# Optimization experiments

Hardware: AMD Instinct MI355X
Metric: run time of the kernel (lower is better)

## Reference

```python
import jax, jax.numpy as jnp
import numpy as np
from jax import lax

EPS = 1e-8

def _cosine_cost(x, y):
    # 1 - cosine_similarity over feature dim: [B,N,M]
    xn = x / jnp.clip(jnp.linalg.norm(x, axis=-1, keepdims=True), EPS)
    yn = y / jnp.clip(jnp.linalg.norm(y, axis=-1, keepdims=True), EPS)
    return 1.0 - jnp.einsum('bnd,bmd->bnm', xn, yn)

def _dtw_table(cost):
    # cost: [B,N,M] -> cumulative cost tc: [B,N,M]
    # tc[i,j] = cost[i,j] + min(tc[i-1,j-1], tc[i-1,j], tc[i,j-1])
    B, N, M = cost.shape
    row0 = jnp.cumsum(cost[:, 0, :], axis=1)  # [B,M]

    def col_step(left, inp):
        c, pdiag, pup = inp  # each [B]
        v = c + jnp.minimum(jnp.minimum(pdiag, pup), left)
        return v, v

    def row_step(prev, cost_row):
        # prev, cost_row: [B,M]
        first = prev[:, 0] + cost_row[:, 0]  # [B]
        xs = (cost_row[:, 1:].T, prev[:, :-1].T, prev[:, 1:].T)  # [M-1,B]
        _, rest = lax.scan(col_step, first, xs)  # [M-1,B]
        row = jnp.concatenate([first[:, None], rest.T], axis=1)  # [B,M]
        return row, row

    _, rows = lax.scan(row_step, row0, jnp.swapaxes(cost[:, 1:, :], 0, 1))
    tc = jnp.concatenate([row0[:, None, :], jnp.swapaxes(rows, 0, 1)], axis=1)
    return tc

def _backtrack(tc):
    # tc: [N,M] -> 0/1 path matrix [N,M]; tie-break diag > up > left,
    # matching the torch equality-chain order.
    N, M = tc.shape
    path0 = jnp.zeros((N, M), tc.dtype).at[N - 1, M - 1].set(1.0)

    def cond(s):
        i, j, _ = s
        return jnp.logical_and(i > 0, j > 0)

    def body(s):
        i, j, p = s
        a = tc[i - 1, j - 1]
        b = tc[i - 1, j]
        c = tc[i, j - 1]
        diag = jnp.logical_and(a <= b, a <= c)
        up = jnp.logical_and(jnp.logical_not(diag), b <= c)
        ni = jnp.where(jnp.logical_or(diag, up), i - 1, i)
        nj = jnp.where(jnp.logical_or(diag, jnp.logical_not(up)), j - 1, j)
        p = p.at[ni, nj].set(1.0)
        return ni, nj, p

    _, _, p = lax.while_loop(cond, body, (jnp.int32(N - 1), jnp.int32(M - 1), path0))
    return p.at[0, 0].set(1.0)

def setup_inputs() -> dict:
    key = jax.random.key(0)
    kx, ky = jax.random.split(key)
    B, N, M, D = 64, 512, 512, 256
    x = jax.random.normal(kx, (B, N, D), dtype=jnp.float32)
    y = jax.random.normal(ky, (B, M, D), dtype=jnp.float32)
    return {"x": x, "y": y}

def reference(x, y):
    cost = _cosine_cost(x, y)                 # [B,N,M]
    tc = _dtw_table(cost)                     # [B,N,M]
    path = jax.vmap(_backtrack)(tc)           # [B,N,M]
    pos = jax.nn.logsumexp(jnp.sum(cost * path, axis=1), axis=1)  # [B]
    neg = jax.nn.logsumexp(jnp.sum(cost, axis=1), axis=1)         # [B]
    return pos - neg
```

## Files before the change

### kernel.cpp

```cpp
#include <hip/hip_runtime.h>
#include <hip/hip_bf16.h>
#include <stdint.h>

typedef __attribute__((ext_vector_type(8))) short short8v;
typedef __attribute__((ext_vector_type(4))) float float4v;
typedef __attribute__((ext_vector_type(4))) unsigned short ushort4v;
typedef __attribute__((ext_vector_type(4))) unsigned int uint4v;

#define FINF __builtin_huge_valf()
#define BB 64
#define NN 512
#define DD 256
#define TT_SKEW 576


static __device__ __forceinline__ unsigned short f2bf(float f) {
  union { float f; uint32_t u; } a; a.f = f;
  uint32_t r = a.u + 0x7fffu + ((a.u >> 16) & 1u);
  return (unsigned short)(r >> 16);
}
static __device__ __forceinline__ float bf2f(uint16_t v) {
  return __uint_as_float(((uint32_t)v) << 16);
}

__global__ __launch_bounds__(64) void pad_zero_kernel(uint16_t* __restrict__ skew)
{
  const int bid = blockIdx.x;
  const int b = bid >> 7, k = bid & 127;
  const int t   = (k < 64) ? k : (448 + k);
  const int jlo = (k < 64) ? 8 * (t + 1) : 0;
  const int jhi = (k < 64) ? 512 : 8 * (t - 511);
  uint16_t* p = skew + ((size_t)b * TT_SKEW + t) * NN;
  const int j = jlo + (int)threadIdx.x * 8;
  if (j < jhi) *(uint4v*)(p + j) = (uint4v){0u, 0u, 0u, 0u};
}

__global__ __launch_bounds__(256) void norm_cast_kernel(
    const float* __restrict__ x, const float* __restrict__ y,
    uint16_t* __restrict__ xnb, uint16_t* __restrict__ ynb)
{
  const int wave = threadIdx.x >> 6, lane = threadIdx.x & 63;
  const int row = blockIdx.x * 4 + wave;
  const float* src; uint16_t* dst;
  if (row < BB * NN) { src = x + (size_t)row * DD;            dst = xnb + (size_t)row * DD; }
  else               { src = y + (size_t)(row - BB*NN) * DD;  dst = ynb + (size_t)(row - BB*NN) * DD; }
  const float4v v = *(const float4v*)(src + lane * 4);
  float s = v[0]*v[0] + v[1]*v[1] + v[2]*v[2] + v[3]*v[3];
  #pragma unroll
  for (int d = 1; d < 64; d <<= 1) s += __shfl_xor(s, d, 64);
  const float inv = 1.0f / fmaxf(sqrtf(s), 1e-8f);
  ushort4v o;
  o[0] = f2bf(v[0] * inv); o[1] = f2bf(v[1] * inv);
  o[2] = f2bf(v[2] * inv); o[3] = f2bf(v[3] * inv);
  *(ushort4v*)(dst + lane * 4) = o;
}

__global__ __launch_bounds__(256) void gemm_cost_kernel(
    const uint16_t* __restrict__ xnb, const uint16_t* __restrict__ ynb,
    uint16_t* __restrict__ skew)
{
  __shared__ uint16_t As[128 * 32];
  __shared__ uint16_t Bs[128 * 32];
  const int bid = blockIdx.x;
  const int b = bid >> 4, tm = (bid >> 2) & 3, tn = bid & 3;
  const int tid = threadIdx.x, wave = tid >> 6, lane = tid & 63;
  const int wr = wave >> 1, wc = wave & 1;

  const char* Ab = (const char*)(xnb + (size_t)b * NN * DD + (size_t)tm * 128 * DD);
  const char* Bb = (const char*)(ynb + (size_t)b * NN * DD + (size_t)tn * 128 * DD);

  float4v acc[4][4];
  #pragma unroll
  for (int i = 0; i < 4; i++)
    #pragma unroll
    for (int j = 0; j < 4; j++) acc[i][j] = (float4v){0.f, 0.f, 0.f, 0.f};

  const int seg0 = wave * 2;
  const int o0 = seg0 * 1024 + lane * 16;
  const int o1 = o0 + 1024;
  const int r0 = o0 >> 6, c0 = o0 & 63;
  const int r1 = o1 >> 6, c1 = o1 & 63;

  for (int kk = 0; kk < 8; kk++) {
    const int kb = kk * 64;
    __builtin_amdgcn_global_load_lds(
        (const __attribute__((address_space(1))) uint32_t*)(Ab + (size_t)r0 * 512 + kb + c0),
        (__attribute__((address_space(3))) uint32_t*)((char*)As + seg0 * 1024), 16, 0, 0);
    __builtin_amdgcn_global_load_lds(
        (const __attribute__((address_space(1))) uint32_t*)(Ab + (size_t)r1 * 512 + kb + c1),
        (__attribute__((address_space(3))) uint32_t*)((char*)As + (seg0 + 1) * 1024), 16, 0, 0);
    __builtin_amdgcn_global_load_lds(
        (const __attribute__((address_space(1))) uint32_t*)(Bb + (size_t)r0 * 512 + kb + c0),
        (__attribute__((address_space(3))) uint32_t*)((char*)Bs + seg0 * 1024), 16, 0, 0);
    __builtin_amdgcn_global_load_lds(
        (const __attribute__((address_space(1))) uint32_t*)(Bb + (size_t)r1 * 512 + kb + c1),
        (__attribute__((address_space(3))) uint32_t*)((char*)Bs + (seg0 + 1) * 1024), 16, 0, 0);
    __syncthreads();

    short8v af[4], bfr[4];
    #pragma unroll
    for (int mi = 0; mi < 4; mi++) {
      const int rr = wr * 64 + mi * 16 + (lane & 15);
      af[mi] = *(const short8v*)((const char*)As + rr * 64 + (lane >> 4) * 16);
    }
    #pragma unroll
    for (int nj = 0; nj < 4; nj++) {
      const int rr = wc * 64 + nj * 16 + (lane & 15);
      bfr[nj] = *(const short8v*)((const char*)Bs + rr * 64 + (lane >> 4) * 16);
    }
    #pragma unroll
    for (int mi = 0; mi < 4; mi++)
      #pragma unroll
      for (int nj = 0; nj < 4; nj++)
        acc[mi][nj] = __builtin_amdgcn_mfma_f32_16x16x32_bf16(af[mi], bfr[nj], acc[mi][nj], 0, 0, 0);
    __syncthreads();
  }

  uint16_t* Cb = skew + (size_t)b * TT_SKEW * NN;
  #pragma unroll
  for (int mi = 0; mi < 4; mi++)
    #pragma unroll
    for (int nj = 0; nj < 4; nj++) {
      const int cc = tn * 128 + wc * 64 + nj * 16 + (lane & 15);
      const int lg = cc >> 3;
      #pragma unroll
      for (int v = 0; v < 4; v++) {
        const int rr = tm * 128 + wr * 64 + mi * 16 + (lane >> 4) * 4 + v;
        Cb[(size_t)(rr + lg) * NN + cc] = f2bf(1.0f - acc[mi][nj][v]);
      }
    }
}

__global__ __launch_bounds__(256) void neg_lse_kernel(
    const uint16_t* __restrict__ skew, float* __restrict__ negbuf)
{
  __shared__ float sm[8];
  const int b = blockIdx.x, tid = threadIdx.x;
  const int wave = tid >> 6, lane = tid & 63;
  const uint32_t* p = (const uint32_t*)(skew + (size_t)b * TT_SKEW * NN) + tid;
  float s0 = 0.f, s1 = 0.f;
  #pragma unroll 8
  for (int t = 0; t < TT_SKEW; ++t) {
    const uint32_t w = p[t * 256];
    s0 += __uint_as_float(w << 16);
    s1 += __uint_as_float(w & 0xFFFF0000u);
  }
  float m = fmaxf(s0, s1);
  #pragma unroll
  for (int d = 1; d < 64; d <<= 1) m = fmaxf(m, __shfl_xor(m, d, 64));
  if (lane == 0) sm[wave] = m;
  __syncthreads();
  m = fmaxf(fmaxf(sm[0], sm[1]), fmaxf(sm[2], sm[3]));
  float e = expf(s0 - m) + expf(s1 - m);
  #pragma unroll
  for (int d = 1; d < 64; d <<= 1) e += __shfl_xor(e, d, 64);
  if (lane == 0) sm[4 + wave] = e;
  __syncthreads();
  if (tid == 0) negbuf[b] = m + logf(sm[4] + sm[5] + sm[6] + sm[7]);
}

__global__ __launch_bounds__(64, 1) void dtw_kernel(
    const uint16_t* __restrict__ skew, const float* __restrict__ negbuf,
    float* __restrict__ out)
{
  extern __shared__ char lds_raw[];
  const int l = threadIdx.x;
  const int b = blockIdx.x;
  const uint16_t* csk = skew + (size_t)b * TT_SKEW * NN;
  const uint64_t base = (uint64_t)(uintptr_t)csk;

  uint32_t voff = 16u * (uint32_t)l;
  const uint32_t voff_max = 16u * (uint32_t)l + 575u * 1024u;

  uint4v ring[8];
  #pragma unroll
  for (int i = 0; i < 8; ++i) {
    asm volatile("global_load_dwordx4 %0, %1, %2"
                 : "=v"(ring[i]) : "v"(voff), "s"(base) : "memory");
    voff += 1024u;
  }

  float tprev[8];
  #pragma unroll
  for (int c = 0; c < 8; ++c) tprev[c] = FINF;
  float sh_p_carry = FINF, cur_last = FINF;
  uint32_t rlane = (uint32_t)(0 - l);
  const uint32_t lane_dec = ((uint32_t)l) << 2;
  const uint32_t dump_addr = 69632u + (((uint32_t)l) << 1);

  for (int t = 0; t < TT_SKEW; t += 8) {
    #pragma unroll
    for (int u = 0; u < 8; ++u) {
      const int tt = t + u;
      asm volatile("s_waitcnt vmcnt(7)" ::: "memory");
      __builtin_amdgcn_sched_barrier(0);
      const uint4v cur = ring[u];

      float sh_c = __shfl_up(cur_last, 1, 64);
      float sh_p = sh_p_carry;
      if (l == 0) { sh_p = FINF; sh_c = (tt == 0) ? 0.0f : FINF; }
      sh_p_carry = sh_c;
      const bool valid = (rlane < 512u);

      float S[8];
      {
        float c0 = __uint_as_float(cur[0] << 16);
        float c1 = __uint_as_float(cur[0] & 0xFFFF0000u);
        float c2 = __uint_as_float(cur[1] << 16);
        float c3 = __uint_as_float(cur[1] & 0xFFFF0000u);
        float c4 = __uint_as_float(cur[2] << 16);
        float c5 = __uint_as_float(cur[2] & 0xFFFF0000u);
        float c6 = __uint_as_float(cur[3] << 16);
        float c7 = __uint_as_float(cur[3] & 0xFFFF0000u);
        S[0] = c0; S[1] = S[0] + c1; S[2] = S[1] + c2; S[3] = S[2] + c3;
        S[4] = S[3] + c4; S[5] = S[4] + c5; S[6] = S[5] + c6; S[7] = S[6] + c7;
      }
      float dcp[8];
      dcp[0] = sh_p;
      #pragma unroll
      for (int c = 1; c < 8; ++c) dcp[c] = tprev[c - 1];
      float w8[8], PW[8];
      w8[0] = fminf(dcp[0], tprev[0]);
      #pragma unroll
      for (int c = 1; c < 8; ++c) w8[c] = fminf(dcp[c], tprev[c]) - S[c - 1];
      PW[0] = w8[0];
      #pragma unroll
      for (int c = 1; c < 8; ++c) PW[c] = fminf(PW[c - 1], w8[c]);
      float tnv[8];
      #pragma unroll
      for (int c = 0; c < 8; ++c) tnv[c] = fminf(PW[c], sh_c) + S[c];
      float lc[8];
      lc[0] = sh_c;
      #pragma unroll
      for (int c = 1; c < 8; ++c) lc[c] = tnv[c - 1];
      uint32_t word = 0;
      #pragma unroll
      for (int c = 0; c < 8; ++c) {
        const bool diag = dcp[c] <= fminf(tprev[c], lc[c]);
        const uint32_t dd = diag ? 0u : ((tprev[c] <= lc[c]) ? 1u : 2u);
        word |= dd << (2 * c);
      }
      const uint32_t wbyte = ((rlane & ~1u) << 7) | ((rlane & 1u) << 1) | lane_dec;
      const uint32_t waddr = valid ? wbyte : dump_addr;
      *(uint16_t*)(lds_raw + waddr) = (uint16_t)word;
      #pragma unroll
      for (int c = 0; c < 8; ++c) tprev[c] = valid ? tnv[c] : tprev[c];
      cur_last = tprev[7];
      rlane += 1u;

      asm volatile("global_load_dwordx4 %0, %1, %2"
                   : "=v"(ring[u]) : "v"(voff), "s"(base) : "memory");
      voff += 1024u;
      if (voff > voff_max) voff = voff_max;
    }
  }
  asm volatile("s_waitcnt vmcnt(0)" ::: "memory");
  __builtin_amdgcn_sched_barrier(0);

  uint16_t* rlo    = (uint16_t*)(lds_raw + 65536);
  uint16_t* rhi    = (uint16_t*)(lds_raw + 66560);
  float*    colpos = (float*)  (lds_raw + 67584);
  const uint32_t* dec32 = (const uint32_t*)lds_raw;

  for (int r = l; r < NN; r += 64) { rlo[r] = 1; rhi[r] = 0; colpos[r] = 0.0f; }
  __syncthreads();
  if (l == 0) {
    int i = NN - 1, j = NN - 1, hicur = NN - 1;
    int cidx = -1; uint32_t cw = 0;
    while (i > 0 && j > 0) {
      const int widx = (i >> 1) * 64 + (j >> 3);
      if (widx != cidx) { cw = dec32[widx]; cidx = widx; }
      const uint32_t dd = (cw >> (((i & 1) << 4) + ((j & 7) << 1))) & 3u;
      if (dd == 2u) { j--; }
      else {
        rlo[i] = (uint16_t)j; rhi[i] = (uint16_t)hicur;
        i--;
        if (dd == 0u) j--;
        hicur = j;
      }
    }
    rlo[i] = (uint16_t)j; rhi[i] = (uint16_t)hicur;
  }
  __syncthreads();
  for (int r = l; r < NN; r += 64) {
    const int lo = rlo[r], hi = rhi[r];
    for (int j = lo; j <= hi; j++) {
      const float cv = bf2f(csk[(size_t)(r + (j >> 3)) * NN + j]);
      atomicAdd(&colpos[j], cv);
    }
  }
  if (l == 0 && rlo[0] != 0) atomicAdd(&colpos[0], bf2f(csk[0]));
  __syncthreads();

  float mv[8];
  float mx2 = -FINF;
  #pragma unroll
  for (int k = 0; k < 8; k++) { mv[k] = colpos[l + 64 * k]; mx2 = fmaxf(mx2, mv[k]); }
  #pragma unroll
  for (int d = 1; d < 64; d <<= 1) mx2 = fmaxf(mx2, __shfl_xor(mx2, d, 64));
  float se2 = 0.f;
  #pragma unroll
  for (int k = 0; k < 8; k++) se2 += expf(mv[k] - mx2);
  #pragma unroll
  for (int d = 1; d < 64; d <<= 1) se2 += __shfl_xor(se2, d, 64);
  const float pos = mx2 + logf(se2);

  if (l == 0) out[b] = pos - negbuf[b];
}

extern "C" void kernel_launch(void* const* d_in, const int* in_sizes, int n_in,
                              void* d_out, int out_size, void* d_ws, size_t ws_size,
                              hipStream_t stream)
{
  (void)in_sizes; (void)n_in; (void)out_size; (void)ws_size;
  const float* x = (const float*)d_in[0];
  const float* y = (const float*)d_in[1];
  float* out = (float*)d_out;
  char* ws = (char*)d_ws;
  uint16_t* xnb  = (uint16_t*)ws;
  uint16_t* ynb  = (uint16_t*)(ws + (size_t)16777216);
  uint16_t* skew = (uint16_t*)(ws + (size_t)33554432);
  float*  negbuf = (float*)  (ws + (size_t)71303168);

  (void)hipFuncSetAttribute((const void*)dtw_kernel,
                            hipFuncAttributeMaxDynamicSharedMemorySize, 69888);

  pad_zero_kernel<<<8192, 64, 0, stream>>>(skew);
  norm_cast_kernel<<<16384, 256, 0, stream>>>(x, y, xnb, ynb);
  gemm_cost_kernel<<<1024, 256, 0, stream>>>(xnb, ynb, skew);
  neg_lse_kernel<<<64, 256, 0, stream>>>(skew, negbuf);
  dtw_kernel<<<64, 64, 69888, stream>>>(skew, negbuf, out);
}
```

Baseline: 292.6 us.

## Split DTW wavefront across two waves with four columns per lane

The DTW wavefront kernel now runs 128 threads per batch, each lane owning 4 columns instead of 8. The second wave lags by 8 diagonal steps and takes its left boundary from a handoff array in LDS written by lane 63 of the first wave. The cost skew layout changes to match: a shift of 4 columns per row, 640 skewed rows, and updated padding, GEMM store, decision-bit packing and backtrack indexing. The aim is a shorter serial dependency chain per diagonal step. In exchange it adds more diagonal steps and a block barrier every four steps.

```diff
diff --git a/kernel.cpp b/kernel.cpp
--- a/kernel.cpp
+++ b/kernel.cpp
@@ -6,12 +6,13 @@
 typedef __attribute__((ext_vector_type(4))) float float4v;
 typedef __attribute__((ext_vector_type(4))) unsigned short ushort4v;
 typedef __attribute__((ext_vector_type(4))) unsigned int uint4v;
+typedef __attribute__((ext_vector_type(2))) unsigned int uint2v;
 
 #define FINF __builtin_huge_valf()
 #define BB 64
 #define NN 512
 #define DD 256
-#define TT_SKEW 576
+#define TT_SKEW 640
 
 
 static __device__ __forceinline__ unsigned short f2bf(float f) {
@@ -26,13 +27,13 @@
 __global__ __launch_bounds__(64) void pad_zero_kernel(uint16_t* __restrict__ skew)
 {
   const int bid = blockIdx.x;
-  const int b = bid >> 7, k = bid & 127;
-  const int t   = (k < 64) ? k : (448 + k);
-  const int jlo = (k < 64) ? 8 * (t + 1) : 0;
-  const int jhi = (k < 64) ? 512 : 8 * (t - 511);
+  const int b = bid >> 8, k = bid & 255;
+  const int t   = (k < 128) ? k : (384 + k);
+  const int jlo = (k < 128) ? 4 * (k + 1) : 0;
+  const int jhi = (k < 128) ? 512 : 4 * (k - 127);
   uint16_t* p = skew + ((size_t)b * TT_SKEW + t) * NN;
-  const int j = jlo + (int)threadIdx.x * 8;
-  if (j < jhi) *(uint4v*)(p + j) = (uint4v){0u, 0u, 0u, 0u};
+  for (int j = jlo + (int)threadIdx.x * 4; j < jhi; j += 256)
+    *(ushort4v*)(p + j) = (ushort4v){0, 0, 0, 0};
 }
 
 __global__ __launch_bounds__(256) void norm_cast_kernel(
@@ -122,7 +123,7 @@
     #pragma unroll
     for (int nj = 0; nj < 4; nj++) {
       const int cc = tn * 128 + wc * 64 + nj * 16 + (lane & 15);
-      const int lg = cc >> 3;
+      const int lg = cc >> 2;
       #pragma unroll
       for (int v = 0; v < 4; v++) {
         const int rr = tm * 128 + wr * 64 + mi * 16 + (lane >> 4) * 4 + v;
@@ -159,118 +160,113 @@
   if (tid == 0) negbuf[b] = m + logf(sm[4] + sm[5] + sm[6] + sm[7]);
 }
 
-__global__ __launch_bounds__(64, 1) void dtw_kernel(
+__global__ __launch_bounds__(128, 1) void dtw_kernel(
     const uint16_t* __restrict__ skew, const float* __restrict__ negbuf,
     float* __restrict__ out)
 {
   extern __shared__ char lds_raw[];
-  const int l = threadIdx.x;
+  float* hand = (float*)(lds_raw + 69632);
+  const int tid = threadIdx.x;
+  const int wv = tid >> 6, l = tid & 63;
+  const int gidx = tid;
   const int b = blockIdx.x;
   const uint16_t* csk = skew + (size_t)b * TT_SKEW * NN;
   const uint64_t base = (uint64_t)(uintptr_t)csk;
-
-  uint32_t voff = 16u * (uint32_t)l;
-  const uint32_t voff_max = 16u * (uint32_t)l + 575u * 1024u;
-
-  uint4v ring[8];
+  const bool is0 = (l == 0);
+  const bool w1 = (wv == 1);
+  const int delta = wv << 3;
+
+  const uint32_t voff_base = 8u * (uint32_t)gidx;
+  uint2v ring[8];
   #pragma unroll
   for (int i = 0; i < 8; ++i) {
-    asm volatile("global_load_dwordx4 %0, %1, %2"
-                 : "=v"(ring[i]) : "v"(voff), "s"(base) : "memory");
-    voff += 1024u;
-  }
-
-  float tprev[8];
-  #pragma unroll
-  for (int c = 0; c < 8; ++c) tprev[c] = FINF;
-  float sh_p_carry = FINF, cur_last = FINF;
-  uint32_t rlane = (uint32_t)(0 - l);
-  const uint32_t lane_dec = ((uint32_t)l) << 2;
-  const uint32_t dump_addr = 69632u + (((uint32_t)l) << 1);
-
-  for (int t = 0; t < TT_SKEW; t += 8) {
+    const uint32_t vo = voff_base + (uint32_t)i * 1024u;
+    asm volatile("global_load_dwordx2 %0, %1, %2"
+                 : "=v"(ring[i]) : "v"(vo), "s"(base));
+  }
+
+  float tp0 = FINF, tp1 = FINF, tp2 = FINF, tp3 = FINF;
+  float cur_last = FINF, sp_carry = FINF, p_carry = FINF, pref = FINF;
+  const uint32_t dump_addr = 71680u + (((uint32_t)gidx) << 1);
+
+  for (int g0 = 0; g0 < 648; g0 += 8) {
     #pragma unroll
     for (int u = 0; u < 8; ++u) {
-      const int tt = t + u;
-      asm volatile("s_waitcnt vmcnt(7)" ::: "memory");
-      __builtin_amdgcn_sched_barrier(0);
-      const uint4v cur = ring[u];
-
-      float sh_c = __shfl_up(cur_last, 1, 64);
-      float sh_p = sh_p_carry;
-      if (l == 0) { sh_p = FINF; sh_c = (tt == 0) ? 0.0f : FINF; }
-      sh_p_carry = sh_c;
-      const bool valid = (rlane < 512u);
-
-      float S[8];
-      {
-        float c0 = __uint_as_float(cur[0] << 16);
-        float c1 = __uint_as_float(cur[0] & 0xFFFF0000u);
-        float c2 = __uint_as_float(cur[1] << 16);
-        float c3 = __uint_as_float(cur[1] & 0xFFFF0000u);
-        float c4 = __uint_as_float(cur[2] << 16);
-        float c5 = __uint_as_float(cur[2] & 0xFFFF0000u);
-        float c6 = __uint_as_float(cur[3] << 16);
-        float c7 = __uint_as_float(cur[3] & 0xFFFF0000u);
-        S[0] = c0; S[1] = S[0] + c1; S[2] = S[1] + c2; S[3] = S[2] + c3;
-        S[4] = S[3] + c4; S[5] = S[4] + c5; S[6] = S[5] + c6; S[7] = S[6] + c7;
+      if (u == 0 || u == 4) __syncthreads();
+      const int t = g0 + u - delta;
+      if (t >= 0 && t < TT_SKEW) {
+        asm volatile("s_waitcnt vmcnt(7)" : "+v"(ring[u]));
+        const uint2v cur = ring[u];
+
+        const float c0 = __uint_as_float(cur[0] << 16);
+        const float c1 = __uint_as_float(cur[0] & 0xFFFF0000u);
+        const float c2 = __uint_as_float(cur[1] << 16);
+        const float c3 = __uint_as_float(cur[1] & 0xFFFF0000u);
+        const float S0 = c0, S1 = S0 + c1, S2 = S1 + c2, S3 = S2 + c3;
+
+        const float sh_raw = __shfl_up(cur_last, 1, 64);
+        const float ovr_c = w1 ? pref : ((t == 0) ? 0.0f : FINF);
+        const float sh_c = is0 ? ovr_c : sh_raw;
+        const float sh_p = is0 ? (w1 ? p_carry : FINF) : sp_carry;
+        p_carry = ovr_c;
+        sp_carry = sh_c;
+
+        const uint32_t rlane = (uint32_t)(t - gidx);
+        const bool valid = rlane < 512u;
+
+        const float mu0 = fminf(sh_p, tp0), mu1 = fminf(tp0, tp1);
+        const float mu2 = fminf(tp1, tp2), mu3 = fminf(tp2, tp3);
+        const float w0c = mu0, w1c = mu1 - S0, w2c = mu2 - S1, w3c = mu3 - S2;
+        const float PW1 = fminf(w0c, w1c), PW2 = fminf(PW1, w2c), PW3 = fminf(PW2, w3c);
+        const float tn0 = fminf(w0c, sh_c) + S0;
+        const float tn1 = fminf(PW1, sh_c) + S1;
+        const float tn2 = fminf(PW2, sh_c) + S2;
+        const float tn3 = fminf(PW3, sh_c) + S3;
+
+        const uint32_t d0 = (sh_c < mu0) ? 2u : ((tp0 < sh_p) ? 1u : 0u);
+        const uint32_t d1 = (tn0 < mu1) ? 2u : ((tp1 < tp0) ? 1u : 0u);
+        const uint32_t d2 = (tn1 < mu2) ? 2u : ((tp2 < tp1) ? 1u : 0u);
+        const uint32_t d3 = (tn2 < mu3) ? 2u : ((tp3 < tp2) ? 1u : 0u);
+        const uint32_t byte = d0 | (d1 << 2) | (d2 << 4) | (d3 << 6);
+        const uint32_t wbyte = ((rlane & ~1u) << 7) | (((uint32_t)gidx) << 1) | (rlane & 1u);
+        *(uint8_t*)(lds_raw + (valid ? wbyte : dump_addr)) = (uint8_t)byte;
+
+        tp0 = valid ? tn0 : tp0; tp1 = valid ? tn1 : tp1;
+        tp2 = valid ? tn2 : tp2; tp3 = valid ? tn3 : tp3;
+        cur_last = tp3;
+        if (gidx == 63 && valid) hand[rlane] = cur_last;
+
+        {
+          int hidx = t - 63; hidx = (hidx < 0) ? 0 : ((hidx > 511) ? 511 : hidx);
+          pref = hand[hidx];
+        }
+        {
+          const int rrow = (t + 8 < TT_SKEW) ? t + 8 : TT_SKEW - 1;
+          const uint32_t vo = voff_base + ((uint32_t)rrow << 10);
+          asm volatile("global_load_dwordx2 %0, %1, %2"
+                       : "=v"(ring[u]) : "v"(vo), "s"(base));
+        }
       }
-      float dcp[8];
-      dcp[0] = sh_p;
-      #pragma unroll
-      for (int c = 1; c < 8; ++c) dcp[c] = tprev[c - 1];
-      float w8[8], PW[8];
-      w8[0] = fminf(dcp[0], tprev[0]);
-      #pragma unroll
-      for (int c = 1; c < 8; ++c) w8[c] = fminf(dcp[c], tprev[c]) - S[c - 1];
-      PW[0] = w8[0];
-      #pragma unroll
-      for (int c = 1; c < 8; ++c) PW[c] = fminf(PW[c - 1], w8[c]);
-      float tnv[8];
-      #pragma unroll
-      for (int c = 0; c < 8; ++c) tnv[c] = fminf(PW[c], sh_c) + S[c];
-      float lc[8];
-      lc[0] = sh_c;
-      #pragma unroll
-      for (int c = 1; c < 8; ++c) lc[c] = tnv[c - 1];
-      uint32_t word = 0;
-      #pragma unroll
-      for (int c = 0; c < 8; ++c) {
-        const bool diag = dcp[c] <= fminf(tprev[c], lc[c]);
-        const uint32_t dd = diag ? 0u : ((tprev[c] <= lc[c]) ? 1u : 2u);
-        word |= dd << (2 * c);
-      }
-      const uint32_t wbyte = ((rlane & ~1u) << 7) | ((rlane & 1u) << 1) | lane_dec;
-      const uint32_t waddr = valid ? wbyte : dump_addr;
-      *(uint16_t*)(lds_raw + waddr) = (uint16_t)word;
-      #pragma unroll
-      for (int c = 0; c < 8; ++c) tprev[c] = valid ? tnv[c] : tprev[c];
-      cur_last = tprev[7];
-      rlane += 1u;
-
-      asm volatile("global_load_dwordx4 %0, %1, %2"
-                   : "=v"(ring[u]) : "v"(voff), "s"(base) : "memory");
-      voff += 1024u;
-      if (voff > voff_max) voff = voff_max;
     }
   }
   asm volatile("s_waitcnt vmcnt(0)" ::: "memory");
-  __builtin_amdgcn_sched_barrier(0);
+  __syncthreads();
 
   uint16_t* rlo    = (uint16_t*)(lds_raw + 65536);
   uint16_t* rhi    = (uint16_t*)(lds_raw + 66560);
   float*    colpos = (float*)  (lds_raw + 67584);
+  float*    red    = (float*)  (lds_raw + 71680);
   const uint32_t* dec32 = (const uint32_t*)lds_raw;
 
-  for (int r = l; r < NN; r += 64) { rlo[r] = 1; rhi[r] = 0; colpos[r] = 0.0f; }
-  __syncthreads();
-  if (l == 0) {
+  for (int r = tid; r < NN; r += 128) { rlo[r] = 1; rhi[r] = 0; colpos[r] = 0.0f; }
+  __syncthreads();
+  if (tid == 0) {
     int i = NN - 1, j = NN - 1, hicur = NN - 1;
     int cidx = -1; uint32_t cw = 0;
     while (i > 0 && j > 0) {
       const int widx = (i >> 1) * 64 + (j >> 3);
       if (widx != cidx) { cw = dec32[widx]; cidx = widx; }
-      const uint32_t dd = (cw >> (((i & 1) << 4) + ((j & 7) << 1))) & 3u;
+      const uint32_t dd = (cw >> ((((j >> 2) & 1) << 4) + ((i & 1) << 3) + ((j & 3) << 1))) & 3u;
       if (dd == 2u) { j--; }
       else {
         rlo[i] = (uint16_t)j; rhi[i] = (uint16_t)hicur;
@@ -282,30 +278,33 @@
     rlo[i] = (uint16_t)j; rhi[i] = (uint16_t)hicur;
   }
   __syncthreads();
-  for (int r = l; r < NN; r += 64) {
+  for (int r = tid; r < NN; r += 128) {
     const int lo = rlo[r], hi = rhi[r];
     for (int j = lo; j <= hi; j++) {
-      const float cv = bf2f(csk[(size_t)(r + (j >> 3)) * NN + j]);
+      const float cv = bf2f(csk[(size_t)(r + (j >> 2)) * NN + j]);
       atomicAdd(&colpos[j], cv);
     }
   }
-  if (l == 0 && rlo[0] != 0) atomicAdd(&colpos[0], bf2f(csk[0]));
-  __syncthreads();
-
-  float mv[8];
+  if (tid == 0 && rlo[0] != 0) atomicAdd(&colpos[0], bf2f(csk[0]));
+  __syncthreads();
+
   float mx2 = -FINF;
-  #pragma unroll
-  for (int k = 0; k < 8; k++) { mv[k] = colpos[l + 64 * k]; mx2 = fmaxf(mx2, mv[k]); }
+  float mv[4];
+  #pragma unroll
+  for (int k = 0; k < 4; k++) { mv[k] = colpos[tid + 128 * k]; mx2 = fmaxf(mx2, mv[k]); }
   #pragma unroll
   for (int d = 1; d < 64; d <<= 1) mx2 = fmaxf(mx2, __shfl_xor(mx2, d, 64));
+  if (l == 0) red[wv] = mx2;
+  __syncthreads();
+  mx2 = fmaxf(red[0], red[1]);
   float se2 = 0.f;
   #pragma unroll
-  for (int k = 0; k < 8; k++) se2 += expf(mv[k] - mx2);
+  for (int k = 0; k < 4; k++) se2 += expf(mv[k] - mx2);
   #pragma unroll
   for (int d = 1; d < 64; d <<= 1) se2 += __shfl_xor(se2, d, 64);
-  const float pos = mx2 + logf(se2);
-
-  if (l == 0) out[b] = pos - negbuf[b];
+  if (l == 0) red[2 + wv] = se2;
+  __syncthreads();
+  if (tid == 0) out[b] = mx2 + logf(red[2] + red[3]) - negbuf[b];
 }
 
 extern "C" void kernel_launch(void* const* d_in, const int* in_sizes, int n_in,
@@ -320,14 +319,14 @@
   uint16_t* xnb  = (uint16_t*)ws;
   uint16_t* ynb  = (uint16_t*)(ws + (size_t)16777216);
   uint16_t* skew = (uint16_t*)(ws + (size_t)33554432);
-  float*  negbuf = (float*)  (ws + (size_t)71303168);
+  float*  negbuf = (float*)  (ws + (size_t)75497472);
 
   (void)hipFuncSetAttribute((const void*)dtw_kernel,
-                            hipFuncAttributeMaxDynamicSharedMemorySize, 69888);
-
-  pad_zero_kernel<<<8192, 64, 0, stream>>>(skew);
+                            hipFuncAttributeMaxDynamicSharedMemorySize, 72192);
+
+  pad_zero_kernel<<<16384, 64, 0, stream>>>(skew);
   norm_cast_kernel<<<16384, 256, 0, stream>>>(x, y, xnb, ynb);
   gemm_cost_kernel<<<1024, 256, 0, stream>>>(xnb, ynb, skew);
   neg_lse_kernel<<<64, 256, 0, stream>>>(skew, negbuf);
-  dtw_kernel<<<64, 64, 69888, stream>>>(skew, negbuf, out);
-}
+  dtw_kernel<<<64, 128, 72192, stream>>>(skew, negbuf, out);
+}
```

After: 301.4 us. 3.0% more time.

## Process two DTW rows per lane step with a 2-row skewed layout and split kernels

Applied to the files above, without the earlier changes.

Changes the skewed cost layout so each lane's column block is offset by two rows instead of one. Each lane then advances two anti-diagonal rows per wavefront step, so the serial forward loop runs about half as many steps (320 instead of 576) with twice the work per step. The DTW kernel is also split into a forward kernel, which writes decision bits to global memory, and a separate backtrack kernel. This adds a global round-trip for the decision table, an extra launch, and a larger skew buffer with more padding to zero.

```diff
diff --git a/kernel.cpp b/kernel.cpp
--- a/kernel.cpp
+++ b/kernel.cpp
@@ -11,7 +11,7 @@
 #define BB 64
 #define NN 512
 #define DD 256
-#define TT_SKEW 576
+#define TT_SKEW 640
 
 
 static __device__ __forceinline__ unsigned short f2bf(float f) {
@@ -25,14 +25,12 @@
 
 __global__ __launch_bounds__(64) void pad_zero_kernel(uint16_t* __restrict__ skew)
 {
-  const int bid = blockIdx.x;
-  const int b = bid >> 7, k = bid & 127;
-  const int t   = (k < 64) ? k : (448 + k);
-  const int jlo = (k < 64) ? 8 * (t + 1) : 0;
-  const int jhi = (k < 64) ? 512 : 8 * (t - 511);
-  uint16_t* p = skew + ((size_t)b * TT_SKEW + t) * NN;
-  const int j = jlo + (int)threadIdx.x * 8;
-  if (j < jhi) *(uint4v*)(p + j) = (uint4v){0u, 0u, 0u, 0u};
+  const int tau = blockIdx.x, b = blockIdx.y, g = threadIdx.x;
+  const int r = tau - 2 * g;
+  if (r < 0 || r > 511) {
+    uint16_t* p = skew + ((size_t)b * TT_SKEW + tau) * NN + g * 8;
+    *(uint4v*)p = (uint4v){0u, 0u, 0u, 0u};
+  }
 }
 
 __global__ __launch_bounds__(256) void norm_cast_kernel(
@@ -126,7 +124,7 @@
       #pragma unroll
       for (int v = 0; v < 4; v++) {
         const int rr = tm * 128 + wr * 64 + mi * 16 + (lane >> 4) * 4 + v;
-        Cb[(size_t)(rr + lg) * NN + cc] = f2bf(1.0f - acc[mi][nj][v]);
+        Cb[(size_t)(rr + 2 * lg) * NN + cc] = f2bf(1.0f - acc[mi][nj][v]);
       }
     }
 }
@@ -159,111 +157,152 @@
   if (tid == 0) negbuf[b] = m + logf(sm[4] + sm[5] + sm[6] + sm[7]);
 }
 
-__global__ __launch_bounds__(64, 1) void dtw_kernel(
-    const uint16_t* __restrict__ skew, const float* __restrict__ negbuf,
-    float* __restrict__ out)
+__global__ __launch_bounds__(64, 1) void dtw_fwd_kernel(
+    const uint16_t* __restrict__ skew, uint32_t* __restrict__ decg)
 {
   extern __shared__ char lds_raw[];
   const int l = threadIdx.x;
   const int b = blockIdx.x;
   const uint16_t* csk = skew + (size_t)b * TT_SKEW * NN;
   const uint64_t base = (uint64_t)(uintptr_t)csk;
-
-  uint32_t voff = 16u * (uint32_t)l;
-  const uint32_t voff_max = 16u * (uint32_t)l + 575u * 1024u;
-
-  uint4v ring[8];
+  const bool is0 = (l == 0);
+  const uint32_t voff_base = 16u * (uint32_t)l;
+
+  uint4v ringA[8], ringB[8];
   #pragma unroll
   for (int i = 0; i < 8; ++i) {
-    asm volatile("global_load_dwordx4 %0, %1, %2"
-                 : "=v"(ring[i]) : "v"(voff), "s"(base) : "memory");
-    voff += 1024u;
-  }
-
-  float tprev[8];
-  #pragma unroll
-  for (int c = 0; c < 8; ++c) tprev[c] = FINF;
-  float sh_p_carry = FINF, cur_last = FINF;
-  uint32_t rlane = (uint32_t)(0 - l);
-  const uint32_t lane_dec = ((uint32_t)l) << 2;
-  const uint32_t dump_addr = 69632u + (((uint32_t)l) << 1);
-
-  for (int t = 0; t < TT_SKEW; t += 8) {
+    const uint32_t voA = voff_base + ((uint32_t)(2 * i) << 10);
+    const uint32_t voB = voA + 1024u;
+    asm volatile("global_load_dwordx4 %0, %1, %2" : "=v"(ringA[i]) : "v"(voA), "s"(base));
+    asm volatile("global_load_dwordx4 %0, %1, %2" : "=v"(ringB[i]) : "v"(voB), "s"(base));
+  }
+
+  float tp[8];
+  #pragma unroll
+  for (int c = 0; c < 8; ++c) tp[c] = FINF;
+  float cl0 = FINF, cl1 = FINF, carry = FINF;
+  const uint32_t dump_addr = 65536u + (((uint32_t)l) << 2);
+
+  for (int t0 = 0; t0 < 320; t0 += 8) {
     #pragma unroll
     for (int u = 0; u < 8; ++u) {
-      const int tt = t + u;
-      asm volatile("s_waitcnt vmcnt(7)" ::: "memory");
-      __builtin_amdgcn_sched_barrier(0);
-      const uint4v cur = ring[u];
-
-      float sh_c = __shfl_up(cur_last, 1, 64);
-      float sh_p = sh_p_carry;
-      if (l == 0) { sh_p = FINF; sh_c = (tt == 0) ? 0.0f : FINF; }
-      sh_p_carry = sh_c;
-      const bool valid = (rlane < 512u);
-
-      float S[8];
+      const int t = t0 + u;
+      float shA = __shfl_up(cl0, 1, 64);
+      float shB = __shfl_up(cl1, 1, 64);
+      if (is0) { shA = (t == 0) ? 0.0f : FINF; shB = FINF; }
+      const float sh_p0 = carry;
+      carry = shB;
+
+      asm volatile("s_waitcnt vmcnt(14)" : "+v"(ringA[u]), "+v"(ringB[u]));
+      const uint4v A = ringA[u];
+      const uint4v Bv = ringB[u];
+
+      const uint32_t rlane = (uint32_t)(t - l);
+      const bool valid = rlane < 256u;
+
+      float ca[8], cbv[8], S0[8], S1[8];
+      #pragma unroll
+      for (int k = 0; k < 4; ++k) {
+        ca[2*k]   = __uint_as_float(A[k] << 16);
+        ca[2*k+1] = __uint_as_float(A[k] & 0xFFFF0000u);
+        cbv[2*k]   = __uint_as_float(Bv[k] << 16);
+        cbv[2*k+1] = __uint_as_float(Bv[k] & 0xFFFF0000u);
+      }
+      S0[0] = ca[0]; S1[0] = cbv[0];
+      #pragma unroll
+      for (int c = 1; c < 8; ++c) { S0[c] = S0[c-1] + ca[c]; S1[c] = S1[c-1] + cbv[c]; }
+
+      float dcp0[8], mu0[8], w0[8], PW0[8], tn0[8];
+      dcp0[0] = sh_p0;
+      #pragma unroll
+      for (int c = 1; c < 8; ++c) dcp0[c] = tp[c-1];
+      #pragma unroll
+      for (int c = 0; c < 8; ++c) mu0[c] = fminf(dcp0[c], tp[c]);
+      w0[0] = mu0[0];
+      #pragma unroll
+      for (int c = 1; c < 8; ++c) w0[c] = mu0[c] - S0[c-1];
+      PW0[0] = w0[0];
+      #pragma unroll
+      for (int c = 1; c < 8; ++c) PW0[c] = fminf(PW0[c-1], w0[c]);
+      #pragma unroll
+      for (int c = 0; c < 8; ++c) tn0[c] = fminf(PW0[c], shA) + S0[c];
+
+      float dcp1[8], mu1[8], w1[8], PW1[8], tn1[8];
+      dcp1[0] = shA;
+      #pragma unroll
+      for (int c = 1; c < 8; ++c) dcp1[c] = tn0[c-1];
+      #pragma unroll
+      for (int c = 0; c < 8; ++c) mu1[c] = fminf(dcp1[c], tn0[c]);
+      w1[0] = mu1[0];
+      #pragma unroll
+      for (int c = 1; c < 8; ++c) w1[c] = mu1[c] - S1[c-1];
+      PW1[0] = w1[0];
+      #pragma unroll
+      for (int c = 1; c < 8; ++c) PW1[c] = fminf(PW1[c-1], w1[c]);
+      #pragma unroll
+      for (int c = 0; c < 8; ++c) tn1[c] = fminf(PW1[c], shB) + S1[c];
+
+      uint32_t word = 0;
       {
-        float c0 = __uint_as_float(cur[0] << 16);
-        float c1 = __uint_as_float(cur[0] & 0xFFFF0000u);
-        float c2 = __uint_as_float(cur[1] << 16);
-        float c3 = __uint_as_float(cur[1] & 0xFFFF0000u);
-        float c4 = __uint_as_float(cur[2] << 16);
-        float c5 = __uint_as_float(cur[2] & 0xFFFF0000u);
-        float c6 = __uint_as_float(cur[3] << 16);
-        float c7 = __uint_as_float(cur[3] & 0xFFFF0000u);
-        S[0] = c0; S[1] = S[0] + c1; S[2] = S[1] + c2; S[3] = S[2] + c3;
-        S[4] = S[3] + c4; S[5] = S[4] + c5; S[6] = S[5] + c6; S[7] = S[6] + c7;
-      }
-      float dcp[8];
-      dcp[0] = sh_p;
-      #pragma unroll
-      for (int c = 1; c < 8; ++c) dcp[c] = tprev[c - 1];
-      float w8[8], PW[8];
-      w8[0] = fminf(dcp[0], tprev[0]);
-      #pragma unroll
-      for (int c = 1; c < 8; ++c) w8[c] = fminf(dcp[c], tprev[c]) - S[c - 1];
-      PW[0] = w8[0];
-      #pragma unroll
-      for (int c = 1; c < 8; ++c) PW[c] = fminf(PW[c - 1], w8[c]);
-      float tnv[8];
-      #pragma unroll
-      for (int c = 0; c < 8; ++c) tnv[c] = fminf(PW[c], sh_c) + S[c];
-      float lc[8];
-      lc[0] = sh_c;
-      #pragma unroll
-      for (int c = 1; c < 8; ++c) lc[c] = tnv[c - 1];
-      uint32_t word = 0;
-      #pragma unroll
-      for (int c = 0; c < 8; ++c) {
-        const bool diag = dcp[c] <= fminf(tprev[c], lc[c]);
-        const uint32_t dd = diag ? 0u : ((tprev[c] <= lc[c]) ? 1u : 2u);
-        word |= dd << (2 * c);
-      }
-      const uint32_t wbyte = ((rlane & ~1u) << 7) | ((rlane & 1u) << 1) | lane_dec;
-      const uint32_t waddr = valid ? wbyte : dump_addr;
-      *(uint16_t*)(lds_raw + waddr) = (uint16_t)word;
-      #pragma unroll
-      for (int c = 0; c < 8; ++c) tprev[c] = valid ? tnv[c] : tprev[c];
-      cur_last = tprev[7];
-      rlane += 1u;
-
-      asm volatile("global_load_dwordx4 %0, %1, %2"
-                   : "=v"(ring[u]) : "v"(voff), "s"(base) : "memory");
-      voff += 1024u;
-      if (voff > voff_max) voff = voff_max;
+        float lc0[8], lc1[8];
+        lc0[0] = shA; lc1[0] = shB;
+        #pragma unroll
+        for (int c = 1; c < 8; ++c) { lc0[c] = tn0[c-1]; lc1[c] = tn1[c-1]; }
+        #pragma unroll
+        for (int c = 0; c < 8; ++c) {
+          const uint32_t e0 = (tp[c] < dcp0[c]) ? 1u : 0u;
+          const uint32_t d0 = (lc0[c] < mu0[c]) ? 2u : e0;
+          const uint32_t e1 = (tn0[c] < dcp1[c]) ? 1u : 0u;
+          const uint32_t d1 = (lc1[c] < mu1[c]) ? 2u : e1;
+          word |= (d0 << (2 * c)) | (d1 << (16 + 2 * c));
+        }
+      }
+      const uint32_t waddr = valid ? ((rlane << 8) | (((uint32_t)l) << 2)) : dump_addr;
+      *(uint32_t*)(lds_raw + waddr) = word;
+
+      #pragma unroll
+      for (int c = 0; c < 8; ++c) tp[c] = valid ? tn1[c] : tp[c];
+      cl0 = valid ? tn0[7] : cl0;
+      cl1 = tp[7];
+
+      {
+        int rr = 2 * (t + 8); if (rr > 638) rr = 638;
+        const uint32_t voA = voff_base + ((uint32_t)rr << 10);
+        const uint32_t voB = voA + 1024u;
+        asm volatile("global_load_dwordx4 %0, %1, %2" : "=v"(ringA[u]) : "v"(voA), "s"(base));
+        asm volatile("global_load_dwordx4 %0, %1, %2" : "=v"(ringB[u]) : "v"(voB), "s"(base));
+      }
     }
   }
   asm volatile("s_waitcnt vmcnt(0)" ::: "memory");
-  __builtin_amdgcn_sched_barrier(0);
-
+
+  uint32_t* dg = decg + (size_t)b * 16384;
+  #pragma unroll 4
+  for (int i = 0; i < 64; ++i)
+    *(uint4v*)(dg + i * 256 + l * 4) = *(const uint4v*)(lds_raw + i * 1024 + l * 16);
+}
+
+__global__ __launch_bounds__(64, 1) void dtw_bt_kernel(
+    const uint16_t* __restrict__ skew, const uint32_t* __restrict__ decg,
+    const float* __restrict__ negbuf, float* __restrict__ out)
+{
+  extern __shared__ char lds_raw[];
   uint16_t* rlo    = (uint16_t*)(lds_raw + 65536);
   uint16_t* rhi    = (uint16_t*)(lds_raw + 66560);
   float*    colpos = (float*)  (lds_raw + 67584);
   const uint32_t* dec32 = (const uint32_t*)lds_raw;
 
+  const int l = threadIdx.x;
+  const int b = blockIdx.x;
+  const uint16_t* csk = skew + (size_t)b * TT_SKEW * NN;
+  const uint32_t* dg = decg + (size_t)b * 16384;
+
+  #pragma unroll 4
+  for (int i = 0; i < 64; ++i)
+    *(uint4v*)(lds_raw + i * 1024 + l * 16) = *(const uint4v*)(dg + i * 256 + l * 4);
   for (int r = l; r < NN; r += 64) { rlo[r] = 1; rhi[r] = 0; colpos[r] = 0.0f; }
   __syncthreads();
+
   if (l == 0) {
     int i = NN - 1, j = NN - 1, hicur = NN - 1;
     int cidx = -1; uint32_t cw = 0;
@@ -285,7 +324,7 @@
   for (int r = l; r < NN; r += 64) {
     const int lo = rlo[r], hi = rhi[r];
     for (int j = lo; j <= hi; j++) {
-      const float cv = bf2f(csk[(size_t)(r + (j >> 3)) * NN + j]);
+      const float cv = bf2f(csk[(size_t)(r + 2 * (j >> 3)) * NN + j]);
       atomicAdd(&colpos[j], cv);
     }
   }
@@ -320,14 +359,18 @@
   uint16_t* xnb  = (uint16_t*)ws;
   uint16_t* ynb  = (uint16_t*)(ws + (size_t)16777216);
   uint16_t* skew = (uint16_t*)(ws + (size_t)33554432);
-  float*  negbuf = (float*)  (ws + (size_t)71303168);
-
-  (void)hipFuncSetAttribute((const void*)dtw_kernel,
-                            hipFuncAttributeMaxDynamicSharedMemorySize, 69888);
-
-  pad_zero_kernel<<<8192, 64, 0, stream>>>(skew);
+  float*  negbuf = (float*)  (ws + (size_t)75497472);
+  uint32_t* decg = (uint32_t*)(ws + (size_t)75501568);
+
+  (void)hipFuncSetAttribute((const void*)dtw_fwd_kernel,
+                            hipFuncAttributeMaxDynamicSharedMemorySize, 65792);
+  (void)hipFuncSetAttribute((const void*)dtw_bt_kernel,
+                            hipFuncAttributeMaxDynamicSharedMemorySize, 69632);
+
+  pad_zero_kernel<<<dim3(TT_SKEW, BB), 64, 0, stream>>>(skew);
   norm_cast_kernel<<<16384, 256, 0, stream>>>(x, y, xnb, ynb);
   gemm_cost_kernel<<<1024, 256, 0, stream>>>(xnb, ynb, skew);
   neg_lse_kernel<<<64, 256, 0, stream>>>(skew, negbuf);
-  dtw_kernel<<<64, 64, 69888, stream>>>(skew, negbuf, out);
-}
+  dtw_fwd_kernel<<<64, 64, 65792, stream>>>(skew, decg);
+  dtw_bt_kernel<<<64, 64, 69632, stream>>>(skew, decg, negbuf, out);
+}
```

Measured after the change: 297.9 us. Within noise of the previous version (+1.8%).
